# Kernel tuning notes

Hardware: AMD Instinct MI355X
Metric: run time of the kernel (lower is better)

Reference implementation:

```python
import jax, jax.numpy as jnp
import numpy as np

DRUG_DIM, TARGET_DIM, HEADS, DIM_HEAD = 768, 2560, 8, 96
INNER = HEADS * DIM_HEAD
NEG = -1000000.0
LN_EPS = 1e-5


def setup_inputs() -> dict:
    key = jax.random.key(0)
    ks = jax.random.split(key, 10)
    b, n, m = 16, 256, 1024
    drug = jax.random.normal(ks[0], (b, n, DRUG_DIM), dtype=jnp.float32)
    target = jax.random.normal(ks[1], (b, m, TARGET_DIM), dtype=jnp.float32)
    drug_mask = jax.random.randint(ks[2], (b, n), 0, 2, dtype=jnp.int32)
    pro_mask = jax.random.randint(ks[3], (b, m), 0, 2, dtype=jnp.int32)
    # parameters (torch Linear weight is (out,in); store as (in,out) for x @ W)
    Wq = jax.random.normal(ks[4], (DRUG_DIM, INNER), dtype=jnp.float32) / np.sqrt(DRUG_DIM)
    Wk = jax.random.normal(ks[5], (TARGET_DIM, INNER), dtype=jnp.float32) / np.sqrt(TARGET_DIM)
    Wv = jax.random.normal(ks[6], (TARGET_DIM, INNER), dtype=jnp.float32) / np.sqrt(TARGET_DIM)
    Wo = jax.random.normal(ks[7], (INNER, DRUG_DIM), dtype=jnp.float32) / np.sqrt(INNER)
    bo = jnp.zeros((DRUG_DIM,), dtype=jnp.float32)
    gamma = jnp.ones((DRUG_DIM,), dtype=jnp.float32)
    beta = jnp.zeros((DRUG_DIM,), dtype=jnp.float32)
    return {"drug": drug, "target": target, "drug_mask": drug_mask,
            "pro_mask": pro_mask, "Wq": Wq, "Wk": Wk, "Wv": Wv,
            "Wo": Wo, "bo": bo, "gamma": gamma, "beta": beta}


def reference(drug, target, drug_mask, pro_mask, Wq, Wk, Wv, Wo, bo, gamma, beta):
    b, n, _ = drug.shape
    m = target.shape[1]
    scale = DIM_HEAD ** -0.5
    # projections -> (b, h, len, d)
    q = (drug @ Wq).reshape(b, n, HEADS, DIM_HEAD).transpose(0, 2, 1, 3)
    k = (target @ Wk).reshape(b, m, HEADS, DIM_HEAD).transpose(0, 2, 1, 3)
    v = (target @ Wv).reshape(b, m, HEADS, DIM_HEAD).transpose(0, 2, 1, 3)
    dots = jnp.einsum('bhnd,bhmd->bhnm', q, k) * scale
    # dual mask: positions where drug_mask==0 (rows) OR pro_mask==0 (cols) -> -1e6
    valid = (drug_mask[:, None, :, None] != 0) & (pro_mask[:, None, None, :] != 0)
    masked_dots = jnp.where(valid, dots, NEG)
    attn = jax.nn.softmax(masked_dots, axis=-1)
    out = jnp.einsum('bhnm,bhmd->bhnd', attn, v)
    out = out.transpose(0, 2, 1, 3).reshape(b, n, INNER)
    out = out @ Wo + bo
    # residual + LayerNorm
    x = out + drug
    mu = jnp.mean(x, axis=-1, keepdims=True)
    var = jnp.mean(jnp.square(x - mu), axis=-1, keepdims=True)
    out = (x - mu) * jax.lax.rsqrt(var + LN_EPS) * gamma + beta
    return (out, attn)
```

## Files before the change

kernel.cpp:

```cpp
#include <hip/hip_runtime.h>

typedef short s16x8 __attribute__((ext_vector_type(8)));
typedef float f32x4 __attribute__((ext_vector_type(4)));

__device__ __forceinline__ unsigned short f2bf(float f) {
    unsigned int u = __builtin_bit_cast(unsigned int, f);
    unsigned int r = u + 0x7FFFu + ((u >> 16) & 1u);
    return (unsigned short)(r >> 16);
}

__device__ __forceinline__ void gload16(const unsigned short* g, unsigned short* l) {
    __builtin_amdgcn_global_load_lds(
        (const __attribute__((address_space(1))) unsigned int*)g,
        (__attribute__((address_space(3))) unsigned int*)l, 16, 0, 0);
}

__global__ __launch_bounds__(256) void cvt_bf16(
    const float* __restrict__ in, unsigned short* __restrict__ out, int n) {
    int i = (blockIdx.x * 256 + threadIdx.x) * 8;
    int stride = gridDim.x * 256 * 8;
    for (; i < n; i += stride) {
        float4 a = *reinterpret_cast<const float4*>(in + i);
        float4 b = *reinterpret_cast<const float4*>(in + i + 4);
        uint4 o;
        o.x = (unsigned int)f2bf(a.x) | ((unsigned int)f2bf(a.y) << 16);
        o.y = (unsigned int)f2bf(a.z) | ((unsigned int)f2bf(a.w) << 16);
        o.z = (unsigned int)f2bf(b.x) | ((unsigned int)f2bf(b.y) << 16);
        o.w = (unsigned int)f2bf(b.z) | ((unsigned int)f2bf(b.w) << 16);
        *reinterpret_cast<uint4*>(out + i) = o;
    }
}

__global__ __launch_bounds__(256) void transpose_bf16(
    const float* __restrict__ W, unsigned short* __restrict__ Wt, int K, int N) {
    __shared__ float t[32][33];
    int k0 = blockIdx.x * 32, n0 = blockIdx.y * 32;
    int tid = threadIdx.x;
    int r = tid >> 5, c = tid & 31;
    for (int p = 0; p < 4; ++p)
        t[p * 8 + r][c] = W[(size_t)(k0 + p * 8 + r) * N + n0 + c];
    __syncthreads();
    for (int p = 0; p < 4; ++p)
        Wt[(size_t)(n0 + p * 8 + r) * K + k0 + c] = f2bf(t[c][p * 8 + r]);
}

template <int OUTMODE>
__global__ __launch_bounds__(256) void gemm_a16(
    const unsigned short* __restrict__ A, const unsigned short* __restrict__ Bt,
    int M, int N, int K,
    float* __restrict__ Cf,
    unsigned short* __restrict__ outA, unsigned short* __restrict__ outVt,
    int seqlen) {
    __shared__ __align__(16) unsigned short As[128 * 32];
    __shared__ __align__(16) unsigned short Bs[128 * 32];
    int tid = threadIdx.x, wid = tid >> 6, lane = tid & 63;
    int nb = N / 128;
    int nwg = gridDim.x;
    int bid = blockIdx.x;
    int wg = bid;
    if ((nwg & 7) == 0) wg = (bid & 7) * (nwg >> 3) + (bid >> 3);
    int tm = wg / nb, tn = wg % nb;
    int m0 = tm * 128, n0 = tn * 128;
    int wm = (wid >> 1) * 64, wn = (wid & 1) * 64;
    int lrow = lane & 15, lkc = lane >> 4;

    const unsigned short* gA[2];
    const unsigned short* gB[2];
    unsigned short* lA[2];
    unsigned short* lB[2];
    for (int p = 0; p < 2; ++p) {
        int e = (wid * 2 + p) * 512 + lane * 8;
        int r = e >> 5;
        int ch = (e >> 3) & 3;
        int sc = ch ^ ((r >> 1) & 3);
        gA[p] = A + (size_t)(m0 + r) * K + sc * 8;
        gB[p] = Bt + (size_t)(n0 + r) * K + sc * 8;
        lA[p] = &As[(wid * 2 + p) * 512];
        lB[p] = &Bs[(wid * 2 + p) * 512];
    }
    int offA[4], offB[4];
    for (int i = 0; i < 4; ++i) {
        int ra = wm + i * 16 + lrow;
        offA[i] = ra * 32 + ((lkc ^ ((ra >> 1) & 3)) * 8);
        int rb = wn + i * 16 + lrow;
        offB[i] = rb * 32 + ((lkc ^ ((rb >> 1) & 3)) * 8);
    }

    f32x4 acc[4][4] = {};
    for (int k0 = 0; k0 < K; k0 += 32) {
        __syncthreads();
        gload16(gA[0], lA[0]);
        gload16(gA[1], lA[1]);
        gload16(gB[0], lB[0]);
        gload16(gB[1], lB[1]);
        gA[0] += 32; gA[1] += 32; gB[0] += 32; gB[1] += 32;
        __syncthreads();
        s16x8 af[4], bfv[4];
        for (int i = 0; i < 4; ++i) af[i] = *reinterpret_cast<const s16x8*>(&As[offA[i]]);
        for (int j = 0; j < 4; ++j) bfv[j] = *reinterpret_cast<const s16x8*>(&Bs[offB[j]]);
        for (int i = 0; i < 4; ++i)
            for (int j = 0; j < 4; ++j)
                acc[i][j] = __builtin_amdgcn_mfma_f32_16x16x32_bf16(af[i], bfv[j], acc[i][j], 0, 0, 0);
    }

    int orow4 = (lane >> 4) * 4;
    int bblk = (OUTMODE == 1) ? (m0 / seqlen) : 0;
    for (int i = 0; i < 4; ++i)
        for (int j = 0; j < 4; ++j)
            for (int r = 0; r < 4; ++r) {
                int row = m0 + wm + i * 16 + orow4 + r;
                int col = n0 + wn + j * 16 + lrow;
                float v = acc[i][j][r];
                if constexpr (OUTMODE == 0) {
                    Cf[(size_t)row * N + col] = v;
                } else {
                    int s = row - bblk * seqlen;
                    unsigned short hv = f2bf(v);
                    if (col < 768) {
                        int h = col / 96, d = col - h * 96;
                        outA[(((size_t)(bblk * 8 + h)) * seqlen + s) * 96 + d] = hv;
                    } else {
                        int cc = col - 768;
                        int h = cc / 96, d = cc - h * 96;
                        outVt[(((size_t)(bblk * 8 + h)) * 96 + d) * seqlen + s] = hv;
                    }
                }
            }
}

#define MT 64
__global__ __launch_bounds__(256) void attn_kernel(
    const unsigned short* __restrict__ Qb,
    const unsigned short* __restrict__ Kb,
    const unsigned short* __restrict__ Vt,
    const int* __restrict__ drug_mask,
    const int* __restrict__ pro_mask,
    float* __restrict__ attn_out,
    unsigned short* __restrict__ AO)
{
    constexpr float scale = 0.10206207261596575f;
    __shared__ __align__(16) unsigned short Qs[64][104];
    __shared__ __align__(16) unsigned short Ks[MT][104];
    __shared__ __align__(16) unsigned short Vts[96][MT + 8];
    __shared__ __align__(16) unsigned short Ps[4][16][MT + 8];
    __shared__ float colv[1024];

    int tid = threadIdx.x, wid = tid >> 6, lane = tid & 63;
    int bh = blockIdx.x, nt = blockIdx.y;
    int b = bh >> 3, h = bh & 7;
    const unsigned short* Qg = Qb + (size_t)bh * 256 * 96 + (size_t)nt * 64 * 96;
    const unsigned short* Kg = Kb + (size_t)bh * 1024 * 96;
    const unsigned short* Vg = Vt + (size_t)bh * 96 * 1024;

    for (int idx = tid; idx < 64 * 12; idx += 256) {
        int r = idx / 12, s = idx % 12;
        *reinterpret_cast<uint4*>(&Qs[r][s * 8]) =
            *reinterpret_cast<const uint4*>(&Qg[r * 96 + s * 8]);
    }
    for (int m = tid; m < 1024; m += 256)
        colv[m] = (pro_mask[b * 1024 + m] != 0) ? 1.0f : 0.0f;

    int lrow = lane & 15, lkg = lane >> 4;
    int qrow0 = nt * 64 + wid * 16;
    float rv[4];
    for (int r = 0; r < 4; ++r)
        rv[r] = (drug_mask[b * 256 + qrow0 + lkg * 4 + r] != 0) ? 1.0f : 0.0f;

    __syncthreads();
    s16x8 qa[3];
    for (int kk = 0; kk < 3; ++kk)
        qa[kk] = *reinterpret_cast<const s16x8*>(&Qs[wid * 16 + lrow][kk * 32 + lkg * 8]);

    float mrun[4], srun[4];
    for (int r = 0; r < 4; ++r) { mrun[r] = -3.0e38f; srun[r] = 0.f; }

    for (int mt = 0; mt < 1024; mt += MT) {
        __syncthreads();
        for (int idx = tid; idx < MT * 12; idx += 256) {
            int r = idx / 12, s = idx % 12;
            *reinterpret_cast<uint4*>(&Ks[r][s * 8]) =
                *reinterpret_cast<const uint4*>(&Kg[(size_t)(mt + r) * 96 + s * 8]);
        }
        __syncthreads();
        float sv[MT / 16][4];
        for (int nf = 0; nf < MT / 16; ++nf) {
            f32x4 acc = {};
            for (int kk = 0; kk < 3; ++kk) {
                s16x8 bb = *reinterpret_cast<const s16x8*>(&Ks[nf * 16 + lrow][kk * 32 + lkg * 8]);
                acc = __builtin_amdgcn_mfma_f32_16x16x32_bf16(qa[kk], bb, acc, 0, 0, 0);
            }
            float cv = colv[mt + nf * 16 + lrow];
            for (int r = 0; r < 4; ++r)
                sv[nf][r] = (rv[r] * cv != 0.f) ? acc[r] * scale : -1.0e6f;
        }
        for (int r = 0; r < 4; ++r) {
            float v = sv[0][r];
            for (int nf = 1; nf < MT / 16; ++nf) v = fmaxf(v, sv[nf][r]);
            for (int o = 1; o < 16; o <<= 1) v = fmaxf(v, __shfl_xor(v, o));
            float nm = fmaxf(mrun[r], v);
            float ts = 0.f;
            for (int nf = 0; nf < MT / 16; ++nf) ts += __expf(sv[nf][r] - nm);
            for (int o = 1; o < 16; o <<= 1) ts += __shfl_xor(ts, o);
            srun[r] = srun[r] * __expf(mrun[r] - nm) + ts;
            mrun[r] = nm;
        }
    }
    float sinv[4];
    for (int r = 0; r < 4; ++r) sinv[r] = 1.0f / srun[r];

    f32x4 oacc[6] = {};
    for (int mt = 0; mt < 1024; mt += MT) {
        __syncthreads();
        for (int idx = tid; idx < MT * 12; idx += 256) {
            int r = idx / 12, s = idx % 12;
            *reinterpret_cast<uint4*>(&Ks[r][s * 8]) =
                *reinterpret_cast<const uint4*>(&Kg[(size_t)(mt + r) * 96 + s * 8]);
        }
        for (int idx = tid; idx < 96 * (MT / 8); idx += 256) {
            int r = idx / (MT / 8), s = idx % (MT / 8);
            *reinterpret_cast<uint4*>(&Vts[r][s * 8]) =
                *reinterpret_cast<const uint4*>(&Vg[(size_t)r * 1024 + mt + s * 8]);
        }
        __syncthreads();
        for (int nf = 0; nf < MT / 16; ++nf) {
            f32x4 acc = {};
            for (int kk = 0; kk < 3; ++kk) {
                s16x8 bb = *reinterpret_cast<const s16x8*>(&Ks[nf * 16 + lrow][kk * 32 + lkg * 8]);
                acc = __builtin_amdgcn_mfma_f32_16x16x32_bf16(qa[kk], bb, acc, 0, 0, 0);
            }
            float cv = colv[mt + nf * 16 + lrow];
            for (int r = 0; r < 4; ++r) {
                float sel = (rv[r] * cv != 0.f) ? acc[r] * scale : -1.0e6f;
                float p = __expf(sel - mrun[r]) * sinv[r];
                attn_out[((size_t)bh * 256 + qrow0 + lkg * 4 + r) * 1024 + mt + nf * 16 + lrow] = p;
                Ps[wid][lkg * 4 + r][nf * 16 + lrow] = f2bf(p);
            }
        }
        __syncthreads();
        for (int kk = 0; kk < MT / 32; ++kk) {
            s16x8 pa = *reinterpret_cast<const s16x8*>(&Ps[wid][lrow][kk * 32 + lkg * 8]);
            for (int df = 0; df < 6; ++df) {
                s16x8 vb = *reinterpret_cast<const s16x8*>(&Vts[df * 16 + lrow][kk * 32 + lkg * 8]);
                oacc[df] = __builtin_amdgcn_mfma_f32_16x16x32_bf16(pa, vb, oacc[df], 0, 0, 0);
            }
        }
    }
    for (int df = 0; df < 6; ++df)
        for (int r = 0; r < 4; ++r) {
            int grow = b * 256 + qrow0 + lkg * 4 + r;
            int gcol = h * 96 + df * 16 + lrow;
            AO[(size_t)grow * 768 + gcol] = f2bf(oacc[df][r]);
        }
}

__global__ __launch_bounds__(256) void ln_kernel(
    const float* __restrict__ O, const float* __restrict__ drug,
    const float* __restrict__ bo, const float* __restrict__ gamma,
    const float* __restrict__ beta, float* __restrict__ out) {
    int row = blockIdx.x, tid = threadIdx.x;
    __shared__ float red[4];
    float x[3], s = 0.f;
    for (int i = 0; i < 3; ++i) {
        int j = tid + i * 256;
        x[i] = O[(size_t)row * 768 + j] + bo[j] + drug[(size_t)row * 768 + j];
        s += x[i];
    }
    for (int o = 32; o; o >>= 1) s += __shfl_xor(s, o);
    if ((tid & 63) == 0) red[tid >> 6] = s;
    __syncthreads();
    float mu = (red[0] + red[1] + red[2] + red[3]) * (1.0f / 768.0f);
    float v = 0.f;
    for (int i = 0; i < 3; ++i) { float d = x[i] - mu; v += d * d; }
    for (int o = 32; o; o >>= 1) v += __shfl_xor(v, o);
    __syncthreads();
    if ((tid & 63) == 0) red[tid >> 6] = v;
    __syncthreads();
    float var = (red[0] + red[1] + red[2] + red[3]) * (1.0f / 768.0f);
    float rs = rsqrtf(var + 1e-5f);
    for (int i = 0; i < 3; ++i) {
        int j = tid + i * 256;
        out[(size_t)row * 768 + j] = (x[i] - mu) * rs * gamma[j] + beta[j];
    }
}

extern "C" void kernel_launch(void* const* d_in, const int* in_sizes, int n_in,
                              void* d_out, int out_size, void* d_ws, size_t ws_size,
                              hipStream_t stream) {
    const float* drug   = (const float*)d_in[0];
    const float* target = (const float*)d_in[1];
    const int*   dmask  = (const int*)d_in[2];
    const int*   pmask  = (const int*)d_in[3];
    const float* Wq = (const float*)d_in[4];
    const float* Wk = (const float*)d_in[5];
    const float* Wv = (const float*)d_in[6];
    const float* Wo = (const float*)d_in[7];
    const float* bo = (const float*)d_in[8];
    const float* gm = (const float*)d_in[9];
    const float* bt = (const float*)d_in[10];

    char* w = (char*)d_ws;
    unsigned short* Wtq  = (unsigned short*)(w + 0);
    unsigned short* Wtkv = (unsigned short*)(w + 1179648);
    unsigned short* Wto  = (unsigned short*)(w + 9043968);
    unsigned short* Qb   = (unsigned short*)(w + 10223616);
    unsigned short* Kb   = (unsigned short*)(w + 16515072);
    unsigned short* Vtb  = (unsigned short*)(w + 41680896);
    unsigned short* AO   = (unsigned short*)(w + 66846720);
    float*          Otmp = (float*)(w + 73138176);
    unsigned short* drugb = (unsigned short*)(w + 85721088);

    float* out_ln   = (float*)d_out;
    float* attn_out = (float*)d_out + 3145728;
    unsigned short* targetb = (unsigned short*)attn_out;

    cvt_bf16<<<2048, 256, 0, stream>>>(target, targetb, 41943040);
    cvt_bf16<<<512, 256, 0, stream>>>(drug, drugb, 3145728);

    transpose_bf16<<<dim3(24, 24), 256, 0, stream>>>(Wq, Wtq, 768, 768);
    transpose_bf16<<<dim3(80, 24), 256, 0, stream>>>(Wk, Wtkv, 2560, 768);
    transpose_bf16<<<dim3(80, 24), 256, 0, stream>>>(Wv, Wtkv + (size_t)768 * 2560, 2560, 768);
    transpose_bf16<<<dim3(24, 24), 256, 0, stream>>>(Wo, Wto, 768, 768);

    gemm_a16<1><<<1536, 256, 0, stream>>>(targetb, Wtkv, 16384, 1536, 2560,
                                          nullptr, Kb, Vtb, 1024);
    gemm_a16<1><<<192, 256, 0, stream>>>(drugb, Wtq, 4096, 768, 768,
                                         nullptr, Qb, nullptr, 256);
    attn_kernel<<<dim3(128, 4), 256, 0, stream>>>(Qb, Kb, Vtb, dmask, pmask, attn_out, AO);
    gemm_a16<0><<<192, 256, 0, stream>>>(AO, Wto, 4096, 768, 768,
                                         Otmp, nullptr, nullptr, 256);
    ln_kernel<<<4096, 256, 0, stream>>>(Otmp, drug, bo, gm, bt, out_ln);
}
```

Measured before the change: 394.7 us.

## Double-buffer GEMM LDS tiles with BK=64 and read K/V directly from global in attention

Result: no change. 390.1 us (-1.2%).

```diff
diff --git a/kernel.cpp b/kernel.cpp
--- a/kernel.cpp
+++ b/kernel.cpp
@@ -13,6 +13,10 @@
     __builtin_amdgcn_global_load_lds(
         (const __attribute__((address_space(1))) unsigned int*)g,
         (__attribute__((address_space(3))) unsigned int*)l, 16, 0, 0);
+}
+
+__device__ __forceinline__ s16x8 ldf(const unsigned short* p) {
+    return *reinterpret_cast<const s16x8*>(p);
 }
 
 __global__ __launch_bounds__(256) void cvt_bf16(
@@ -45,62 +49,85 @@
 }
 
 template <int OUTMODE>
-__global__ __launch_bounds__(256) void gemm_a16(
+__global__ __launch_bounds__(256, 2) void gemm_db(
     const unsigned short* __restrict__ A, const unsigned short* __restrict__ Bt,
     int M, int N, int K,
     float* __restrict__ Cf,
     unsigned short* __restrict__ outA, unsigned short* __restrict__ outVt,
     int seqlen) {
-    __shared__ __align__(16) unsigned short As[128 * 32];
-    __shared__ __align__(16) unsigned short Bs[128 * 32];
+    extern __shared__ __align__(16) unsigned short smem[];
+    unsigned short* As = smem;
+    unsigned short* Bs = smem + 16384;
+
     int tid = threadIdx.x, wid = tid >> 6, lane = tid & 63;
     int nb = N / 128;
-    int nwg = gridDim.x;
-    int bid = blockIdx.x;
-    int wg = bid;
-    if ((nwg & 7) == 0) wg = (bid & 7) * (nwg >> 3) + (bid >> 3);
+    int nwg = gridDim.x, bid = blockIdx.x;
+    int wg = (bid & 7) * (nwg >> 3) + (bid >> 3);
     int tm = wg / nb, tn = wg % nb;
     int m0 = tm * 128, n0 = tn * 128;
     int wm = (wid >> 1) * 64, wn = (wid & 1) * 64;
     int lrow = lane & 15, lkc = lane >> 4;
 
-    const unsigned short* gA[2];
-    const unsigned short* gB[2];
-    unsigned short* lA[2];
-    unsigned short* lB[2];
-    for (int p = 0; p < 2; ++p) {
-        int e = (wid * 2 + p) * 512 + lane * 8;
-        int r = e >> 5;
-        int ch = (e >> 3) & 3;
-        int sc = ch ^ ((r >> 1) & 3);
-        gA[p] = A + (size_t)(m0 + r) * K + sc * 8;
-        gB[p] = Bt + (size_t)(n0 + r) * K + sc * 8;
-        lA[p] = &As[(wid * 2 + p) * 512];
-        lB[p] = &Bs[(wid * 2 + p) * 512];
-    }
-    int offA[4], offB[4];
-    for (int i = 0; i < 4; ++i) {
-        int ra = wm + i * 16 + lrow;
-        offA[i] = ra * 32 + ((lkc ^ ((ra >> 1) & 3)) * 8);
-        int rb = wn + i * 16 + lrow;
-        offB[i] = rb * 32 + ((lkc ^ ((rb >> 1) & 3)) * 8);
-    }
-
+    int lrsub = lane >> 3;
+    int gch = (lane & 7) ^ lrsub;
+    const unsigned short* gA[4];
+    const unsigned short* gB[4];
+    unsigned short* lA[4];
+    unsigned short* lB[4];
+#pragma unroll
+    for (int p = 0; p < 4; ++p) {
+        int r = (wid * 4 + p) * 8 + lrsub;
+        gA[p] = A + (size_t)(m0 + r) * K + gch * 8;
+        gB[p] = Bt + (size_t)(n0 + r) * K + gch * 8;
+        lA[p] = As + (wid * 4 + p) * 512;
+        lB[p] = Bs + (wid * 4 + p) * 512;
+    }
+
+    int offA[2][4], offB[2][4];
+#pragma unroll
+    for (int kh = 0; kh < 2; ++kh)
+#pragma unroll
+        for (int i = 0; i < 4; ++i) {
+            int ra = wm + i * 16 + lrow;
+            offA[kh][i] = ra * 64 + (((kh * 4 + lkc) ^ (ra & 7)) * 8);
+            int rb = wn + i * 16 + lrow;
+            offB[kh][i] = rb * 64 + (((kh * 4 + lkc) ^ (rb & 7)) * 8);
+        }
+
+    int NT = K / 64;
     f32x4 acc[4][4] = {};
-    for (int k0 = 0; k0 < K; k0 += 32) {
+
+#pragma unroll
+    for (int p = 0; p < 4; ++p) { gload16(gA[p], lA[p]); gload16(gB[p], lB[p]); }
+
+    int cur = 0;
+    for (int t = 0; t < NT; ++t) {
         __syncthreads();
-        gload16(gA[0], lA[0]);
-        gload16(gA[1], lA[1]);
-        gload16(gB[0], lB[0]);
-        gload16(gB[1], lB[1]);
-        gA[0] += 32; gA[1] += 32; gB[0] += 32; gB[1] += 32;
-        __syncthreads();
-        s16x8 af[4], bfv[4];
-        for (int i = 0; i < 4; ++i) af[i] = *reinterpret_cast<const s16x8*>(&As[offA[i]]);
-        for (int j = 0; j < 4; ++j) bfv[j] = *reinterpret_cast<const s16x8*>(&Bs[offB[j]]);
-        for (int i = 0; i < 4; ++i)
-            for (int j = 0; j < 4; ++j)
-                acc[i][j] = __builtin_amdgcn_mfma_f32_16x16x32_bf16(af[i], bfv[j], acc[i][j], 0, 0, 0);
+        if (t + 1 < NT) {
+            int nxt = (cur ^ 1) * 8192;
+            int koff = (t + 1) * 64;
+#pragma unroll
+            for (int p = 0; p < 4; ++p) {
+                gload16(gA[p] + koff, lA[p] + nxt);
+                gload16(gB[p] + koff, lB[p] + nxt);
+            }
+        }
+        const unsigned short* Ab = As + cur * 8192;
+        const unsigned short* Bb = Bs + cur * 8192;
+#pragma unroll
+        for (int kh = 0; kh < 2; ++kh) {
+            s16x8 af[4], bfv[4];
+#pragma unroll
+            for (int i = 0; i < 4; ++i) af[i] = ldf(&Ab[offA[kh][i]]);
+#pragma unroll
+            for (int j = 0; j < 4; ++j) bfv[j] = ldf(&Bb[offB[kh][j]]);
+#pragma unroll
+            for (int i = 0; i < 4; ++i)
+#pragma unroll
+                for (int j = 0; j < 4; ++j)
+                    acc[i][j] = __builtin_amdgcn_mfma_f32_16x16x32_bf16(af[i], bfv[j], acc[i][j], 0, 0, 0);
+        }
+        cur ^= 1;
     }
 
     int orow4 = (lane >> 4) * 4;
@@ -140,8 +167,6 @@
 {
     constexpr float scale = 0.10206207261596575f;
     __shared__ __align__(16) unsigned short Qs[64][104];
-    __shared__ __align__(16) unsigned short Ks[MT][104];
-    __shared__ __align__(16) unsigned short Vts[96][MT + 8];
     __shared__ __align__(16) unsigned short Ps[4][16][MT + 8];
     __shared__ float colv[1024];
 
@@ -169,36 +194,35 @@
     __syncthreads();
     s16x8 qa[3];
     for (int kk = 0; kk < 3; ++kk)
-        qa[kk] = *reinterpret_cast<const s16x8*>(&Qs[wid * 16 + lrow][kk * 32 + lkg * 8]);
+        qa[kk] = ldf(&Qs[wid * 16 + lrow][kk * 32 + lkg * 8]);
 
     float mrun[4], srun[4];
     for (int r = 0; r < 4; ++r) { mrun[r] = -3.0e38f; srun[r] = 0.f; }
 
     for (int mt = 0; mt < 1024; mt += MT) {
-        __syncthreads();
-        for (int idx = tid; idx < MT * 12; idx += 256) {
-            int r = idx / 12, s = idx % 12;
-            *reinterpret_cast<uint4*>(&Ks[r][s * 8]) =
-                *reinterpret_cast<const uint4*>(&Kg[(size_t)(mt + r) * 96 + s * 8]);
-        }
-        __syncthreads();
         float sv[MT / 16][4];
+#pragma unroll
         for (int nf = 0; nf < MT / 16; ++nf) {
             f32x4 acc = {};
+#pragma unroll
             for (int kk = 0; kk < 3; ++kk) {
-                s16x8 bb = *reinterpret_cast<const s16x8*>(&Ks[nf * 16 + lrow][kk * 32 + lkg * 8]);
+                s16x8 bb = ldf(Kg + (size_t)(mt + nf * 16 + lrow) * 96 + kk * 32 + lkg * 8);
                 acc = __builtin_amdgcn_mfma_f32_16x16x32_bf16(qa[kk], bb, acc, 0, 0, 0);
             }
             float cv = colv[mt + nf * 16 + lrow];
+#pragma unroll
             for (int r = 0; r < 4; ++r)
                 sv[nf][r] = (rv[r] * cv != 0.f) ? acc[r] * scale : -1.0e6f;
         }
+#pragma unroll
         for (int r = 0; r < 4; ++r) {
             float v = sv[0][r];
+#pragma unroll
             for (int nf = 1; nf < MT / 16; ++nf) v = fmaxf(v, sv[nf][r]);
             for (int o = 1; o < 16; o <<= 1) v = fmaxf(v, __shfl_xor(v, o));
             float nm = fmaxf(mrun[r], v);
             float ts = 0.f;
+#pragma unroll
             for (int nf = 0; nf < MT / 16; ++nf) ts += __expf(sv[nf][r] - nm);
             for (int o = 1; o < 16; o <<= 1) ts += __shfl_xor(ts, o);
             srun[r] = srun[r] * __expf(mrun[r] - nm) + ts;
@@ -210,25 +234,16 @@
 
     f32x4 oacc[6] = {};
     for (int mt = 0; mt < 1024; mt += MT) {
-        __syncthreads();
-        for (int idx = tid; idx < MT * 12; idx += 256) {
-            int r = idx / 12, s = idx % 12;
-            *reinterpret_cast<uint4*>(&Ks[r][s * 8]) =
-                *reinterpret_cast<const uint4*>(&Kg[(size_t)(mt + r) * 96 + s * 8]);
-        }
-        for (int idx = tid; idx < 96 * (MT / 8); idx += 256) {
-            int r = idx / (MT / 8), s = idx % (MT / 8);
-            *reinterpret_cast<uint4*>(&Vts[r][s * 8]) =
-                *reinterpret_cast<const uint4*>(&Vg[(size_t)r * 1024 + mt + s * 8]);
-        }
-        __syncthreads();
+#pragma unroll
         for (int nf = 0; nf < MT / 16; ++nf) {
             f32x4 acc = {};
+#pragma unroll
             for (int kk = 0; kk < 3; ++kk) {
-                s16x8 bb = *reinterpret_cast<const s16x8*>(&Ks[nf * 16 + lrow][kk * 32 + lkg * 8]);
+                s16x8 bb = ldf(Kg + (size_t)(mt + nf * 16 + lrow) * 96 + kk * 32 + lkg * 8);
                 acc = __builtin_amdgcn_mfma_f32_16x16x32_bf16(qa[kk], bb, acc, 0, 0, 0);
             }
             float cv = colv[mt + nf * 16 + lrow];
+#pragma unroll
             for (int r = 0; r < 4; ++r) {
                 float sel = (rv[r] * cv != 0.f) ? acc[r] * scale : -1.0e6f;
                 float p = __expf(sel - mrun[r]) * sinv[r];
@@ -236,14 +251,19 @@
                 Ps[wid][lkg * 4 + r][nf * 16 + lrow] = f2bf(p);
             }
         }
-        __syncthreads();
+        asm volatile("s_waitcnt lgkmcnt(0)" ::: "memory");
+        __builtin_amdgcn_sched_barrier(0);
+#pragma unroll
         for (int kk = 0; kk < MT / 32; ++kk) {
-            s16x8 pa = *reinterpret_cast<const s16x8*>(&Ps[wid][lrow][kk * 32 + lkg * 8]);
+            s16x8 pa = ldf(&Ps[wid][lrow][kk * 32 + lkg * 8]);
+#pragma unroll
             for (int df = 0; df < 6; ++df) {
-                s16x8 vb = *reinterpret_cast<const s16x8*>(&Vts[df * 16 + lrow][kk * 32 + lkg * 8]);
+                s16x8 vb = ldf(Vg + (size_t)(df * 16 + lrow) * 1024 + mt + kk * 32 + lkg * 8);
                 oacc[df] = __builtin_amdgcn_mfma_f32_16x16x32_bf16(pa, vb, oacc[df], 0, 0, 0);
             }
         }
+        asm volatile("s_waitcnt lgkmcnt(0)" ::: "memory");
+        __builtin_amdgcn_sched_barrier(0);
     }
     for (int df = 0; df < 6; ++df)
         for (int r = 0; r < 4; ++r) {
@@ -321,12 +341,12 @@
     transpose_bf16<<<dim3(80, 24), 256, 0, stream>>>(Wv, Wtkv + (size_t)768 * 2560, 2560, 768);
     transpose_bf16<<<dim3(24, 24), 256, 0, stream>>>(Wo, Wto, 768, 768);
 
-    gemm_a16<1><<<1536, 256, 0, stream>>>(targetb, Wtkv, 16384, 1536, 2560,
-                                          nullptr, Kb, Vtb, 1024);
-    gemm_a16<1><<<192, 256, 0, stream>>>(drugb, Wtq, 4096, 768, 768,
-                                         nullptr, Qb, nullptr, 256);
+    gemm_db<1><<<1536, 256, 65536, stream>>>(targetb, Wtkv, 16384, 1536, 2560,
+                                             nullptr, Kb, Vtb, 1024);
+    gemm_db<1><<<192, 256, 65536, stream>>>(drugb, Wtq, 4096, 768, 768,
+                                            nullptr, Qb, nullptr, 256);
     attn_kernel<<<dim3(128, 4), 256, 0, stream>>>(Qb, Kb, Vtb, dmask, pmask, attn_out, AO);
-    gemm_a16<0><<<192, 256, 0, stream>>>(AO, Wto, 4096, 768, 768,
-                                         Otmp, nullptr, nullptr, 256);
+    gemm_db<0><<<192, 256, 65536, stream>>>(AO, Wto, 4096, 768, 768,
+                                            Otmp, nullptr, nullptr, 256);
     ln_kernel<<<4096, 256, 0, stream>>>(Otmp, drug, bo, gm, bt, out_ln);
 }
```
